# Kernel optimization log

Measured on AMD Instinct MI355X. Metric: run time of the kernel, lower is better.

## Reference

```python
import jax, jax.numpy as jnp
import numpy as np


def setup_inputs() -> dict:
    key = jax.random.key(0)
    k1, k2 = jax.random.split(key)
    B, N, C = 8, 65536, 64
    npoint, nsample = 16384, 32
    features = jax.random.normal(k1, (B, N, C), dtype=jnp.float32)
    coarse_map = jax.random.randint(k2, (B, npoint, nsample), 0, N, dtype=jnp.int32)
    return {"features": features, "coarse_map": coarse_map}


def reference(features, coarse_map):
    # features: [B, N, C]; coarse_map: [B, npoint, nsample] indices into N
    B = features.shape[0]
    # gather neighbors: [B, npoint, nsample, C]
    grouped = features[jnp.arange(B)[:, None, None], coarse_map]
    # max pool over neighbors -> [B, npoint, C]
    return jnp.max(grouped, axis=2)
```

## Files before the change

kernel.cpp:

```cpp
#include <hip/hip_runtime.h>
#include <math.h>

constexpr int B  = 8;
constexpr int N  = 65536;
constexpr int C  = 64;
constexpr int NP = 16384;
constexpr int NS = 32;
constexpr int C4 = C / 4;

__global__ __launch_bounds__(256) void gather_max_kernel(
    const float4* __restrict__ feat,
    const int*    __restrict__ cmap,
    float4*       __restrict__ out)
{
    const int tid   = blockIdx.x * blockDim.x + threadIdx.x;
    const int point = tid >> 4;
    const int j     = tid & 15;
    if (point >= B * NP) return;

    const int    b        = point >> 14;
    const size_t featBase = (size_t)b * N * C4;

    const int2 myIdx = ((const int2*)(cmap + (size_t)point * NS))[j];

    const int lane  = threadIdx.x & 63;
    const int gbase = lane & ~15;

    float4 m = make_float4(-INFINITY, -INFINITY, -INFINITY, -INFINITY);
#pragma unroll
    for (int s = 0; s < NS; ++s) {
        const int v   = (s & 1) ? myIdx.y : myIdx.x;
        const int idx = __shfl(v, gbase + (s >> 1), 64);
        const float4 f = feat[featBase + (size_t)idx * C4 + j];
        m.x = fmaxf(m.x, f.x);
        m.y = fmaxf(m.y, f.y);
        m.z = fmaxf(m.z, f.z);
        m.w = fmaxf(m.w, f.w);
    }

    out[(size_t)point * C4 + j] = m;
}

extern "C" void kernel_launch(void* const* d_in, const int* in_sizes, int n_in,
                              void* d_out, int out_size, void* d_ws, size_t ws_size,
                              hipStream_t stream) {
    const float4* feat = (const float4*)d_in[0];
    const int*    cmap = (const int*)d_in[1];
    float4*       out  = (float4*)d_out;

    const int totalThreads = B * NP * 16;
    const int block = 256;
    const int grid  = (totalThreads + block - 1) / block;
    gather_max_kernel<<<grid, block, 0, stream>>>(feat, cmap, out);
}
```

Measured before the change: 274.1 us.

## Split channel dimension into slices across blocks for gather-max

Each block now handles 128 points but only a 32-byte slice of the channels, with two threads per point, and consecutive blocks cover the 8 slices of the same point group. This spreads each gathered 256-byte row across several blocks so the concurrently running blocks touch fewer distinct rows, which aims to improve cache locality. In exchange, each point's index list is re-read 8 times and every gather access is only 32 bytes wide, giving less coalescing per wavefront.

```diff
diff --git a/kernel.cpp b/kernel.cpp
--- a/kernel.cpp
+++ b/kernel.cpp
@@ -8,37 +8,48 @@
 constexpr int NS = 32;
 constexpr int C4 = C / 4;
 
-__global__ __launch_bounds__(256) void gather_max_kernel(
+constexpr int SLICES = 8;
+constexpr int PTS_PER_BLOCK = 128;
+
+__global__ __launch_bounds__(256) void gather_max_sliced(
     const float4* __restrict__ feat,
     const int*    __restrict__ cmap,
     float4*       __restrict__ out)
 {
-    const int tid   = blockIdx.x * blockDim.x + threadIdx.x;
-    const int point = tid >> 4;
-    const int j     = tid & 15;
-    if (point >= B * NP) return;
+    const int slice  = blockIdx.x & (SLICES - 1);
+    const int pblock = blockIdx.x >> 3;
+    const int p      = threadIdx.x >> 1;
+    const int j      = threadIdx.x & 1;
+    const int point  = pblock * PTS_PER_BLOCK + p;
 
     const int    b        = point >> 14;
-    const size_t featBase = (size_t)b * N * C4;
+    const size_t rowBase  = (size_t)b * N * C4;
+    const int    sliceOff = slice * 2;
 
-    const int2 myIdx = ((const int2*)(cmap + (size_t)point * NS))[j];
+    int q[16];
+    const int4* cp = (const int4*)(cmap + (size_t)point * NS);
+#pragma unroll
+    for (int k = 0; k < 4; ++k) {
+        const int4 t = cp[j * 4 + k];
+        q[4 * k + 0] = t.x; q[4 * k + 1] = t.y;
+        q[4 * k + 2] = t.z; q[4 * k + 3] = t.w;
+    }
 
-    const int lane  = threadIdx.x & 63;
-    const int gbase = lane & ~15;
+    const int lane     = threadIdx.x & 63;
+    const int pairBase = lane & ~1;
 
     float4 m = make_float4(-INFINITY, -INFINITY, -INFINITY, -INFINITY);
 #pragma unroll
     for (int s = 0; s < NS; ++s) {
-        const int v   = (s & 1) ? myIdx.y : myIdx.x;
-        const int idx = __shfl(v, gbase + (s >> 1), 64);
-        const float4 f = feat[featBase + (size_t)idx * C4 + j];
+        const int idx = __shfl(q[s & 15], pairBase + (s >> 4), 64);
+        const float4 f = feat[rowBase + (size_t)idx * C4 + sliceOff + j];
         m.x = fmaxf(m.x, f.x);
         m.y = fmaxf(m.y, f.y);
         m.z = fmaxf(m.z, f.z);
         m.w = fmaxf(m.w, f.w);
     }
 
-    out[(size_t)point * C4 + j] = m;
+    out[(size_t)point * C4 + sliceOff + j] = m;
 }
 
 extern "C" void kernel_launch(void* const* d_in, const int* in_sizes, int n_in,
@@ -48,8 +59,7 @@
     const int*    cmap = (const int*)d_in[1];
     float4*       out  = (float4*)d_out;
 
-    const int totalThreads = B * NP * 16;
-    const int block = 256;
-    const int grid  = (totalThreads + block - 1) / block;
-    gather_max_kernel<<<grid, block, 0, stream>>>(feat, cmap, out);
+    const int pblocks = (B * NP) / PTS_PER_BLOCK;
+    const int grid    = pblocks * SLICES;
+    gather_max_sliced<<<grid, 256, 0, stream>>>(feat, cmap, out);
 }
```

Measured after the change: 531.5 us. +93.9%, slower.

## Convert features to fp16 in workspace and gather-max at half precision

Applied to the files above, without the earlier changes.

Adds a pass that converts the fp32 feature table to fp16 in the workspace, then runs a gather-max kernel that reads 128-byte half rows with 8 threads per point. The aim is to halve the bytes moved by the random neighbor gathers. The cost is an extra streaming conversion pass each call, plus rounding error in the outputs from the fp16 storage. If the workspace is too small, it falls back to the original fp32 kernel.

```diff
diff --git a/kernel.cpp b/kernel.cpp
--- a/kernel.cpp
+++ b/kernel.cpp
@@ -1,4 +1,5 @@
 #include <hip/hip_runtime.h>
+#include <hip/hip_fp16.h>
 #include <math.h>
 
 constexpr int B  = 8;
@@ -6,50 +7,109 @@
 constexpr int C  = 64;
 constexpr int NP = 16384;
 constexpr int NS = 32;
+constexpr size_t FEAT_ELEMS = (size_t)B * N * C;
+constexpr size_t HALF_BYTES = FEAT_ELEMS * 2;
+
+static __device__ __forceinline__ __half2 h2max(__half2 a, __half2 b) {
+    __half2 r;
+    r.x = __hmax(a.x, b.x);
+    r.y = __hmax(a.y, b.y);
+    return r;
+}
+
+__global__ __launch_bounds__(256) void convert_f32_to_f16(
+    const float4* __restrict__ src, uint2* __restrict__ dst)
+{
+    const int i = blockIdx.x * 256 + threadIdx.x;
+    const float4 v = src[i];
+    const __half2 a = __floats2half2_rn(v.x, v.y);
+    const __half2 b = __floats2half2_rn(v.z, v.w);
+    uint2 o;
+    o.x = *(const unsigned int*)&a;
+    o.y = *(const unsigned int*)&b;
+    dst[i] = o;
+}
+
+__global__ __launch_bounds__(256) void gather_max_f16(
+    const uint4* __restrict__ featH,
+    const int*   __restrict__ cmap,
+    float4*      __restrict__ out)
+{
+    const int tid   = blockIdx.x * 256 + threadIdx.x;
+    const int point = tid >> 3;
+    const int j     = tid & 7;
+    const int b     = point >> 14;
+    const size_t rowBase = (size_t)b * N * 8;
+
+    const int4 q = ((const int4*)(cmap + (size_t)point * NS))[j];
+
+    const int lane  = threadIdx.x & 63;
+    const int gbase = lane & ~7;
+
+    const __half2 ninf = __float2half2_rn(-INFINITY);
+    __half2 m0 = ninf, m1 = ninf, m2 = ninf, m3 = ninf;
+
+#pragma unroll
+    for (int s = 0; s < NS; ++s) {
+        const int v = (s & 3) == 0 ? q.x : (s & 3) == 1 ? q.y
+                    : (s & 3) == 2 ? q.z : q.w;
+        const int idx = __shfl(v, gbase + (s >> 2), 64);
+        const uint4 u = featH[rowBase + (size_t)idx * 8 + j];
+        m0 = h2max(m0, *(const __half2*)&u.x);
+        m1 = h2max(m1, *(const __half2*)&u.y);
+        m2 = h2max(m2, *(const __half2*)&u.z);
+        m3 = h2max(m3, *(const __half2*)&u.w);
+    }
+
+    const float2 f0 = __half22float2(m0), f1 = __half22float2(m1);
+    const float2 f2 = __half22float2(m2), f3 = __half22float2(m3);
+    out[(size_t)point * 16 + j * 2 + 0] = make_float4(f0.x, f0.y, f1.x, f1.y);
+    out[(size_t)point * 16 + j * 2 + 1] = make_float4(f2.x, f2.y, f3.x, f3.y);
+}
+
 constexpr int C4 = C / 4;
-
-__global__ __launch_bounds__(256) void gather_max_kernel(
-    const float4* __restrict__ feat,
-    const int*    __restrict__ cmap,
-    float4*       __restrict__ out)
+__global__ __launch_bounds__(256) void gather_max_f32(
+    const float4* __restrict__ feat, const int* __restrict__ cmap,
+    float4* __restrict__ out)
 {
     const int tid   = blockIdx.x * blockDim.x + threadIdx.x;
     const int point = tid >> 4;
     const int j     = tid & 15;
-    if (point >= B * NP) return;
-
     const int    b        = point >> 14;
     const size_t featBase = (size_t)b * N * C4;
-
     const int2 myIdx = ((const int2*)(cmap + (size_t)point * NS))[j];
-
     const int lane  = threadIdx.x & 63;
     const int gbase = lane & ~15;
-
     float4 m = make_float4(-INFINITY, -INFINITY, -INFINITY, -INFINITY);
 #pragma unroll
     for (int s = 0; s < NS; ++s) {
         const int v   = (s & 1) ? myIdx.y : myIdx.x;
         const int idx = __shfl(v, gbase + (s >> 1), 64);
         const float4 f = feat[featBase + (size_t)idx * C4 + j];
-        m.x = fmaxf(m.x, f.x);
-        m.y = fmaxf(m.y, f.y);
-        m.z = fmaxf(m.z, f.z);
-        m.w = fmaxf(m.w, f.w);
+        m.x = fmaxf(m.x, f.x); m.y = fmaxf(m.y, f.y);
+        m.z = fmaxf(m.z, f.z); m.w = fmaxf(m.w, f.w);
     }
-
     out[(size_t)point * C4 + j] = m;
 }
 
 extern "C" void kernel_launch(void* const* d_in, const int* in_sizes, int n_in,
                               void* d_out, int out_size, void* d_ws, size_t ws_size,
                               hipStream_t stream) {
-    const float4* feat = (const float4*)d_in[0];
-    const int*    cmap = (const int*)d_in[1];
-    float4*       out  = (float4*)d_out;
+    const int* cmap = (const int*)d_in[1];
+    float4*    out  = (float4*)d_out;
 
-    const int totalThreads = B * NP * 16;
-    const int block = 256;
-    const int grid  = (totalThreads + block - 1) / block;
-    gather_max_kernel<<<grid, block, 0, stream>>>(feat, cmap, out);
+    if (ws_size >= HALF_BYTES) {
+        const float4* src = (const float4*)d_in[0];
+        uint2* dst = (uint2*)d_ws;
+        const int convBlocks = (int)(FEAT_ELEMS / 4 / 256);
+        convert_f32_to_f16<<<convBlocks, 256, 0, stream>>>(src, dst);
+
+        const int threads = B * NP * 8;
+        gather_max_f16<<<threads / 256, 256, 0, stream>>>(
+            (const uint4*)d_ws, cmap, out);
+    } else {
+        const float4* feat = (const float4*)d_in[0];
+        const int threads = B * NP * 16;
+        gather_max_f32<<<threads / 256, 256, 0, stream>>>(feat, cmap, out);
+    }
 }
```

Result: slower. 290.4 us (+5.9%).
